# Kernel tuning notes

Measured on AMD Instinct MI355X. Metric: run time of the kernel, lower is better.

The kernel has to match this reference:

```python
import jax, jax.numpy as jnp
import numpy as np
from jax import lax

B, E, DIN = 16, 1024, 128   # batch, num_edges, link_state_dim
P, D = 2048, 128            # num_paths, path_state_dim


def _topology():
    # deterministic ragged paths: lengths in [4,16], at least one of max length 16
    lengths = 4 + (np.arange(P) % 13)
    idx = np.repeat(np.arange(P), lengths).astype(np.int32)          # path id per entry
    seqs = np.concatenate([np.arange(l) for l in lengths]).astype(np.int32)  # position in path
    paths = np.random.RandomState(0).randint(0, E, size=idx.shape[0]).astype(np.int32)
    return paths, idx, seqs


def setup_inputs() -> dict:
    key = jax.random.key(0)
    ks = jax.random.split(key, 8)
    paths, idx, seqs = _topology()
    s_in = 1.0 / np.sqrt(DIN)
    s_h = 1.0 / np.sqrt(D)
    return dict(
        inputs=jax.random.normal(ks[0], (B, E, DIN), jnp.float32),
        W_in=jax.random.normal(ks[1], (DIN, 3 * D), jnp.float32) * s_in,
        W_rec=jax.random.normal(ks[2], (D, 3 * D), jnp.float32) * s_h,
        b_in=jnp.zeros((3 * D,), jnp.float32),
        b_rec=jnp.zeros((3 * D,), jnp.float32),
        wq=jax.random.normal(ks[3], (D, D), jnp.float32) * s_h,
        wk=jax.random.normal(ks[4], (D, D), jnp.float32) * s_h,
        wv=jax.random.normal(ks[5], (D, D), jnp.float32) * s_h,
        paths=paths, idx=idx, seqs=seqs,
    )


def _forward(inputs, W_in, W_rec, b_in, b_rec, wq, wk, wv, paths, idx, seqs, max_len):
    Bc = inputs.shape[0]
    # --- ragged gather -> dense zero-padded tensor [B, P, max_len, DIN] (tf.gather + scatter_nd) ---
    h_tild = inputs[:, paths]                                  # [B, n_entries, DIN]
    link = jnp.zeros((Bc, P, max_len, DIN), inputs.dtype)
    link = link.at[:, idx, seqs].set(h_tild)
    x = link.reshape(Bc * P, max_len, DIN)                     # [BP, L, DIN]
    # --- GRU over time (keras GRUCell default: reset_after=True, tanh/sigmoid) ---
    xg = jnp.einsum('nld,de->lne', x, W_in) + b_in             # [L, BP, 3D]
    h0 = jnp.zeros((Bc * P, D), inputs.dtype)

    def step(h, xg_t):
        hg = h @ W_rec + b_rec                                 # [BP, 3D]
        xz, xr, xh = jnp.split(xg_t, 3, axis=-1)
        hz, hr, hh = jnp.split(hg, 3, axis=-1)
        z = jax.nn.sigmoid(xz + hz)
        r = jax.nn.sigmoid(xr + hr)
        hc = jnp.tanh(xh + r * hh)
        hn = z * h + (1.0 - z) * hc
        return hn, hn

    last, hs = lax.scan(step, h0, xg)                          # last:[BP,D], hs:[L,BP,D]
    hs = jnp.transpose(hs, (1, 0, 2))                          # [BP, L, D]
    # --- single-query QKV attention (raw scores, no softmax, as in source) ---
    key_ = hs @ wk                                             # [BP, L, D]
    val = hs @ wv                                              # [BP, L, D]
    q = last @ wq                                              # [BP, D]
    att = jnp.einsum('nld,nd->nl', key_, q)                    # [BP, L]
    ctx = jnp.einsum('nl,nld->nd', att, val)                   # [BP, D]
    return ctx.reshape(Bc, P, D)


def reference(inputs, W_in, W_rec, b_in, b_rec, wq, wk, wv, paths, idx, seqs):
    max_len = int(np.max(np.asarray(seqs))) + 1                # static (16)
    return _forward(inputs, W_in, W_rec, b_in, b_rec, wq, wk, wv, paths, idx, seqs, max_len)
```

## Files before the change

kernel.cpp:

```cpp
#include <hip/hip_runtime.h>
#include <hip/hip_bf16.h>
#include <cstddef>

#define P_ 2048
#define B_ 16
#define E_ 1024
#define D_ 128
#define L_ 16
#define TD_ 384

#define NEG_L2E (-1.44269504088896340736f)
#define TWO_L2E (2.88539008177792681472f)

typedef _Float16 f16x2 __attribute__((ext_vector_type(2)));
typedef _Float16 f16x8 __attribute__((ext_vector_type(8)));
typedef float    f32x4 __attribute__((ext_vector_type(4)));

__device__ __forceinline__ unsigned short f2h(float x) {
    _Float16 h = (_Float16)x;
    return __builtin_bit_cast(unsigned short, h);
}
__device__ __forceinline__ unsigned pk2(float a, float b) {
    return __builtin_bit_cast(unsigned, __builtin_amdgcn_cvt_pkrtz(a, b));
}
__device__ __forceinline__ float lo16(unsigned u) {
    return (float)__builtin_bit_cast(f16x2, u)[0];
}
__device__ __forceinline__ float hi16(unsigned u) {
    return (float)__builtin_bit_cast(f16x2, u)[1];
}
__device__ __forceinline__ float ex2(float x) {
#if __has_builtin(__builtin_amdgcn_exp2f)
    return __builtin_amdgcn_exp2f(x);
#else
    return exp2f(x);
#endif
}
__device__ __forceinline__ float dot2w(unsigned hu, unsigned qu, float c) {
#if __has_builtin(__builtin_amdgcn_fdot2)
    typedef __fp16 h2v __attribute__((ext_vector_type(2)));
    return __builtin_amdgcn_fdot2(__builtin_bit_cast(h2v, hu),
                                  __builtin_bit_cast(h2v, qu), c, false);
#else
    f16x2 h = __builtin_bit_cast(f16x2, hu), q = __builtin_bit_cast(f16x2, qu);
    return c + (float)h[0] * (float)q[0] + (float)h[1] * (float)q[1];
#endif
}

__device__ __forceinline__ void binv4(const float* __restrict__ d, float* __restrict__ o) {
    float f1 = d[0] * d[1];
    float f2 = f1 * d[2];
    float f3 = f2 * d[3];
    float r  = __builtin_amdgcn_rcpf(f3);
    o[3] = r * f2;
    float t  = r * d[3];
    o[2] = t * f1;
    float u  = t * d[2];
    o[1] = u * d[0];
    o[0] = u * d[1];
}

__device__ __forceinline__ void wf16(const float* __restrict__ src,
                                     unsigned short* __restrict__ dst, int g, int N,
                                     float sc) {
    int lane = g & 63, kt = (g >> 6) & 3, tile = g >> 8;
    int k0 = kt * 32 + (lane >> 4) * 8;
    int c = tile * 16 + (lane & 15);
#pragma unroll
    for (int j = 0; j < 8; ++j)
        dst[(size_t)g * 8 + j] = f2h(src[(size_t)(k0 + j) * N + c] * sc);
}

__device__ __forceinline__ void* hp(void* base, int t, int s, int boff) {
    return (char*)base + ((t * 16 + s) << 8) + (boff ^ ((s & 7) << 4));
}
__device__ __forceinline__ const void* hpc(const void* base, int t, int s, int boff) {
    return (const char*)base + ((t * 16 + s) << 8) + (boff ^ ((s & 7) << 4));
}

__global__ __launch_bounds__(256) void k_prep(const float* __restrict__ W_rec,
                                              const float* __restrict__ W_in,
                                              const float* __restrict__ wq,
                                              const float* __restrict__ wk,
                                              const float* __restrict__ wv,
                                              const int* __restrict__ paths,
                                              int* __restrict__ pt,
                                              unsigned short* __restrict__ WfR,
                                              unsigned short* __restrict__ WfI,
                                              unsigned short* __restrict__ wvf,
                                              float* __restrict__ M) {
    __shared__ float wk_lds[128 * 129];
    __shared__ float wq_row2[2][128];
    int blk = blockIdx.x, tid = threadIdx.x;
    if (blk < 128) {
        int gid = blk * 256 + tid;
        int p = gid >> 4, s = gid & 15;
        int c = p / 13, r = p - c * 13;
        int len = 4 + r;
        int off = 4 * p + 78 * c + (r * (r - 1)) / 2;
        pt[gid] = (s < len) ? paths[off + s] : E_;
        return;
    } else if (blk < 152) {
        int gg = (blk - 128) * 256 + tid;
        wf16(W_rec, WfR, gg, TD_, ((gg >> 8) < 16) ? NEG_L2E : TWO_L2E);
        return;
    } else if (blk < 176) {
        int gg = (blk - 152) * 256 + tid;
        wf16(W_in, WfI, gg, TD_, ((gg >> 8) < 16) ? NEG_L2E : TWO_L2E);
        return;
    } else if (blk < 184) {
        wf16(wv, wvf, (blk - 176) * 256 + tid, 128, 1.f);
        return;
    }
    int j0 = (blk - 184) * 2;
    int d = tid & 127, half = tid >> 7;
    for (int r = half * 64; r < half * 64 + 64; ++r)
        wk_lds[r * 129 + d] = wk[r * 128 + d];
    wq_row2[half][d] = wq[(j0 + half) * 128 + d];
    __syncthreads();
    float acc = 0.f;
    for (int k = 0; k < 128; ++k) acc += wq_row2[half][k] * wk_lds[d * 129 + k];
    M[(j0 + half) * 128 + d] = acc;
}

__global__ __launch_bounds__(256) void k_G(const float* __restrict__ inputs,
                                           const unsigned short* __restrict__ WfI,
                                           const float* __restrict__ b_in,
                                           const float* __restrict__ b_rec,
                                           unsigned short* __restrict__ G2,
                                           const float* __restrict__ M,
                                           unsigned short* __restrict__ Mf) {
    if (blockIdx.x >= 1024) {
        int tb = blockIdx.x - 1024;
        if (tb < 8) {
            wf16(M, Mf, tb * 256 + threadIdx.x, 128, 1.f);
        } else {
            for (int i = threadIdx.x; i < 2048; i += 256) {
                int bx = i >> 7, cc = i & 127;
                size_t base = ((size_t)(bx * (E_ + 1) + E_) * 128 + cc) * 4;
                G2[base]     = f2h((b_in[cc] + b_rec[cc]) * NEG_L2E);
                G2[base + 1] = f2h((b_in[128 + cc] + b_rec[128 + cc]) * NEG_L2E);
                G2[base + 2] = f2h(b_in[256 + cc] * TWO_L2E);
                G2[base + 3] = 0;
            }
        }
        return;
    }
    __shared__ __align__(16) unsigned short a_lds[16][136];
    __shared__ __align__(16) unsigned short g_lds[16][128][4];
    int tid = threadIdx.x, w = tid >> 6, L = tid & 63;
    int l15 = L & 15, q = L >> 4;
    int row0 = blockIdx.x * 16;
    int badd = row0 >> 10;
    {
        int r = tid >> 4, c = (tid & 15) * 8;
        const float4* p = (const float4*)(inputs + (size_t)(row0 + r) * 128 + c);
        float4 v0 = p[0], v1 = p[1];
        uint4 st;
        st.x = pk2(v0.x, v0.y); st.y = pk2(v0.z, v0.w);
        st.z = pk2(v1.x, v1.y); st.w = pk2(v1.z, v1.w);
        *(uint4*)&a_lds[r][c] = st;
    }
    __syncthreads();
    f16x8 af[4];
#pragma unroll
    for (int kt = 0; kt < 4; ++kt)
        af[kt] = *(const f16x8*)&a_lds[l15][kt * 32 + q * 8];
#pragma unroll
    for (int ct = 0; ct < 6; ++ct) {
        int tl = 6 * w + ct;
        f32x4 acc = (f32x4){0.f, 0.f, 0.f, 0.f};
#pragma unroll
        for (int kt = 0; kt < 4; ++kt)
            acc = __builtin_amdgcn_mfma_f32_16x16x32_f16(
                af[kt], *(const f16x8*)(WfI + (size_t)((tl * 4 + kt) * 64 + L) * 8), acc, 0, 0, 0);
        int g  = tl >> 3;
        int dd = (tl & 7) * 16 + l15;
        float sg  = (g < 2) ? NEG_L2E : TWO_L2E;
        float bia = (b_in[tl * 16 + l15] + (g < 2 ? b_rec[tl * 16 + l15] : 0.f)) * sg;
#pragma unroll
        for (int j = 0; j < 4; ++j) {
            int r = q * 4 + j;
            g_lds[r][dd][g] = f2h(acc[j] + bia);
        }
    }
    __syncthreads();
    {
        const uint4* src = (const uint4*)g_lds;
        uint4* dst = (uint4*)(G2 + (size_t)(row0 + badd) * 512);
#pragma unroll
        for (int i = 0; i < 4; ++i) dst[tid + 256 * i] = src[tid + 256 * i];
    }
}

__global__ __launch_bounds__(512, 4) void k_rec(const unsigned short* __restrict__ WfR,
                                                const float* __restrict__ b_rec,
                                                const unsigned short* __restrict__ G2,
                                                const int* __restrict__ pt,
                                                const unsigned short* __restrict__ Mf,
                                                const unsigned short* __restrict__ wvf,
                                                float* __restrict__ out) {
    __shared__ __align__(16) unsigned short hsl[16][16][128];
    __shared__ __align__(16) unsigned short qkb[16][136];
    __shared__ __align__(16) unsigned short svb[16][136];
    __shared__ float attp[2][16][16];
    __shared__ int ofs_lds[16][16];

    int tid = threadIdx.x, w = tid >> 6, L = tid & 63;
    int l15 = L & 15, q = L >> 4;
    int c0 = 16 * w + 4 * q;
    int n0 = blockIdx.x * 16;
    int b  = n0 >> 11;
    int p0 = n0 & (P_ - 1);
    int bb = b * (E_ + 1);

    f16x8 afw[3][4];
#pragma unroll
    for (int g = 0; g < 3; ++g)
#pragma unroll
        for (int kt = 0; kt < 4; ++kt)
            afw[g][kt] = *(const f16x8*)(WfR + (size_t)(((g * 8 + w) * 4 + kt) * 64 + L) * 8);

    if (tid < 256)
        ofs_lds[tid >> 4][tid & 15] = (bb + pt[p0 * L_ + tid]) << 10;

    f32x4 rh4;
#pragma unroll
    for (int j = 0; j < 4; ++j) rh4[j] = b_rec[256 + c0 + j] * TWO_L2E;
    float h_reg[4] = {0.f, 0.f, 0.f, 0.f};
    __syncthreads();

    int ofs[16];
    {
        const uint4* op = (const uint4*)&ofs_lds[l15][0];
        uint4 o0 = op[0], o1 = op[1], o2 = op[2], o3 = op[3];
        ofs[0]  = o0.x; ofs[1]  = o0.y; ofs[2]  = o0.z; ofs[3]  = o0.w;
        ofs[4]  = o1.x; ofs[5]  = o1.y; ofs[6]  = o1.z; ofs[7]  = o1.w;
        ofs[8]  = o2.x; ofs[9]  = o2.y; ofs[10] = o2.z; ofs[11] = o2.w;
        ofs[12] = o3.x; ofs[13] = o3.y; ofs[14] = o3.z; ofs[15] = o3.w;
    }

    const char* g2c = (const char*)G2 + (size_t)c0 * 8;
    uint4 cur0 = *(const uint4*)(g2c + ofs[0]);
    uint4 cur1 = *(const uint4*)(g2c + ofs[0] + 16);

#pragma unroll
    for (int t = 0; t < L_; ++t) {
        uint4 nx0 = cur0, nx1 = cur1;
        if (t < 15) {
            const char* gp = g2c + ofs[t + 1];
            nx0 = *(const uint4*)(gp);
            nx1 = *(const uint4*)(gp + 16);
        }

        float xh[4];
        f32x4 acc[3];
        acc[0][0] = lo16(cur0.x); acc[0][1] = lo16(cur0.z);
        acc[0][2] = lo16(cur1.x); acc[0][3] = lo16(cur1.z);
        acc[1][0] = hi16(cur0.x); acc[1][1] = hi16(cur0.z);
        acc[1][2] = hi16(cur1.x); acc[1][3] = hi16(cur1.z);
        xh[0] = lo16(cur0.y); xh[1] = lo16(cur0.w);
        xh[2] = lo16(cur1.y); xh[3] = lo16(cur1.w);
        acc[2] = rh4;

        if (t > 0) {
            f16x8 hf[4];
#pragma unroll
            for (int kt = 0; kt < 4; ++kt)
                hf[kt] = *(const f16x8*)hpc(hsl, t - 1, l15, kt * 64 + q * 16);
#pragma unroll
            for (int g = 0; g < 3; ++g)
#pragma unroll
                for (int kt = 0; kt < 4; ++kt)
                    acc[g] = __builtin_amdgcn_mfma_f32_16x16x32_f16(afw[g][kt], hf[kt], acc[g], 0, 0, 0);
        }

        float dz[4], dr[4];
#pragma unroll
        for (int j = 0; j < 4; ++j) {
            dz[j] = 1.f + ex2(acc[0][j]);
            dr[j] = 1.f + ex2(acc[1][j]);
        }
        float z4[4], r4[4];
        binv4(dz, z4);
        binv4(dr, r4);
        float dh[4];
#pragma unroll
        for (int j = 0; j < 4; ++j)
            dh[j] = 1.f + ex2(fminf(xh[j] + r4[j] * acc[2][j], 30.f));
        float y4[4];
        binv4(dh, y4);
        float hn[4];
#pragma unroll
        for (int j = 0; j < 4; ++j) {
            float hc = 1.f - 2.f * y4[j];
            hn[j] = hc + z4[j] * (h_reg[j] - hc);
            h_reg[j] = hn[j];
        }
        uint2 st;
        st.x = pk2(hn[0], hn[1]); st.y = pk2(hn[2], hn[3]);
        *(uint2*)hp(hsl, t, l15, c0 * 2) = st;
        cur0 = nx0; cur1 = nx1;

        __builtin_amdgcn_wave_barrier();
        __builtin_amdgcn_s_waitcnt(0xC07F);
        __builtin_amdgcn_s_barrier();
        __builtin_amdgcn_wave_barrier();
    }

    {
        f16x8 hf[4];
#pragma unroll
        for (int kt = 0; kt < 4; ++kt)
            hf[kt] = *(const f16x8*)hpc(hsl, 15, l15, kt * 64 + q * 16);
        f32x4 a = (f32x4){0.f, 0.f, 0.f, 0.f};
#pragma unroll
        for (int kt = 0; kt < 4; ++kt)
            a = __builtin_amdgcn_mfma_f32_16x16x32_f16(
                *(const f16x8*)(Mf + (size_t)((w * 4 + kt) * 64 + L) * 8), hf[kt], a, 0, 0, 0);
        uint2 st;
        st.x = pk2(a[0], a[1]); st.y = pk2(a[2], a[3]);
        *(uint2*)&qkb[l15][c0] = st;
    }
    __syncthreads();

    {
        int s = tid & 15, l = (tid >> 4) & 15, half = tid >> 8;
        const uint4* qr = (const uint4*)&qkb[s][half * 64];
        float a = 0.f;
#pragma unroll
        for (int k8 = 0; k8 < 8; ++k8) {
            uint4 hh = *(const uint4*)hpc(hsl, l, s, half * 128 + k8 * 16);
            uint4 qq = qr[k8];
            a = dot2w(hh.x, qq.x, a); a = dot2w(hh.y, qq.y, a);
            a = dot2w(hh.z, qq.z, a); a = dot2w(hh.w, qq.w, a);
        }
        attp[half][s][l] = a;
    }
    __syncthreads();

    {
        int s = tid >> 5, d0 = (tid & 31) * 4;
        float v[4] = {0.f, 0.f, 0.f, 0.f};
#pragma unroll
        for (int l = 0; l < 16; ++l) {
            float a = attp[0][s][l] + attp[1][s][l];
            uint2 hu = *(const uint2*)hpc(hsl, l, s, d0 * 2);
            v[0] += a * lo16(hu.x); v[1] += a * hi16(hu.x);
            v[2] += a * lo16(hu.y); v[3] += a * hi16(hu.y);
        }
        uint2 st;
        st.x = pk2(v[0], v[1]); st.y = pk2(v[2], v[3]);
        *(uint2*)&svb[s][d0] = st;
    }
    __syncthreads();

    {
        f16x8 sf[4];
#pragma unroll
        for (int kt = 0; kt < 4; ++kt)
            sf[kt] = *(const f16x8*)&svb[l15][kt * 32 + q * 8];
        f32x4 a = (f32x4){0.f, 0.f, 0.f, 0.f};
#pragma unroll
        for (int kt = 0; kt < 4; ++kt)
            a = __builtin_amdgcn_mfma_f32_16x16x32_f16(
                *(const f16x8*)(wvf + (size_t)((w * 4 + kt) * 64 + L) * 8), sf[kt], a, 0, 0, 0);
        *(f32x4*)&out[(size_t)(n0 + l15) * D_ + c0] = a;
    }
}

extern "C" void kernel_launch(void* const* d_in, const int* in_sizes, int n_in,
                              void* d_out, int out_size, void* d_ws, size_t ws_size,
                              hipStream_t stream) {
    const float* inputs = (const float*)d_in[0];
    const float* W_in   = (const float*)d_in[1];
    const float* W_rec  = (const float*)d_in[2];
    const float* b_in   = (const float*)d_in[3];
    const float* b_rec  = (const float*)d_in[4];
    const float* wq     = (const float*)d_in[5];
    const float* wk     = (const float*)d_in[6];
    const float* wvp    = (const float*)d_in[7];
    const int* paths    = (const int*)d_in[8];

    const size_t off_pt  = 0;
    const size_t off_WfR = off_pt  + (size_t)P_ * L_ * 4;
    const size_t off_WfI = off_WfR + (size_t)24 * 256 * 16;
    const size_t off_Mf  = off_WfI + (size_t)24 * 256 * 16;
    const size_t off_wvf = off_Mf  + (size_t)8 * 256 * 16;
    const size_t off_M   = off_wvf + (size_t)8 * 256 * 16;
    const size_t off_G2  = off_M   + (size_t)128 * 128 * 4;
    char* ws = (char*)d_ws;
    int* pt             = (int*)(ws + off_pt);
    unsigned short* WfR = (unsigned short*)(ws + off_WfR);
    unsigned short* WfI = (unsigned short*)(ws + off_WfI);
    unsigned short* Mf  = (unsigned short*)(ws + off_Mf);
    unsigned short* wvf = (unsigned short*)(ws + off_wvf);
    float* M            = (float*)(ws + off_M);
    unsigned short* G2  = (unsigned short*)(ws + off_G2);
    float* out = (float*)d_out;

    k_prep<<<dim3(248), dim3(256), 0, stream>>>(W_rec, W_in, wq, wk, wvp, paths,
                                                pt, WfR, WfI, wvf, M);
    k_G<<<dim3(1024 + 8 + 1), dim3(256), 0, stream>>>(inputs, WfI, b_in, b_rec,
                                                      G2, M, Mf);
    k_rec<<<dim3(B_ * P_ / 16), dim3(512), 0, stream>>>(WfR, b_rec, G2, pt,
                                                        Mf, wvf, out);
}
```

Baseline: 173.6 us.

## Fuse input projection into recurrent kernel, gathering fp16 inputs per step

Removes the separate k_G kernel that precomputed per-edge input gate projections (G2). The prep kernel now converts inputs to an fp16 copy with a zero row per batch for padding, and writes Mf directly in MFMA layout. The recurrent kernel gathers the raw fp16 input rows and computes the input projection with extra MFMAs each step, with biases added in registers. This drops one launch and the G2 round trip, but the sequential loop now does twice the MFMA work and holds both weight sets in registers, which adds register pressure.

```diff
diff --git a/kernel.cpp b/kernel.cpp
--- a/kernel.cpp
+++ b/kernel.cpp
@@ -83,12 +83,14 @@
                                               const float* __restrict__ wq,
                                               const float* __restrict__ wk,
                                               const float* __restrict__ wv,
+                                              const float* __restrict__ inputs,
                                               const int* __restrict__ paths,
                                               int* __restrict__ pt,
                                               unsigned short* __restrict__ WfR,
                                               unsigned short* __restrict__ WfI,
                                               unsigned short* __restrict__ wvf,
-                                              float* __restrict__ M) {
+                                              unsigned short* __restrict__ Mf,
+                                              unsigned short* __restrict__ X2) {
     __shared__ float wk_lds[128 * 129];
     __shared__ float wq_row2[2][128];
     int blk = blockIdx.x, tid = threadIdx.x;
@@ -111,6 +113,20 @@
     } else if (blk < 184) {
         wf16(wv, wvf, (blk - 176) * 256 + tid, 128, 1.f);
         return;
+    } else if (blk >= 248) {
+        int g = (blk - 248) * 16 + (tid >> 4);
+        int seg = tid & 15;
+        int b = g / 1025;
+        int e = g - b * 1025;
+        uint4 st = (uint4){0u, 0u, 0u, 0u};
+        if (e < 1024) {
+            const float4* p = (const float4*)(inputs + (size_t)(g - b) * 128 + seg * 8);
+            float4 v0 = p[0], v1 = p[1];
+            st.x = pk2(v0.x, v0.y); st.y = pk2(v0.z, v0.w);
+            st.z = pk2(v1.x, v1.y); st.w = pk2(v1.z, v1.w);
+        }
+        *(uint4*)(X2 + (size_t)g * 128 + seg * 8) = st;
+        return;
     }
     int j0 = (blk - 184) * 2;
     int d = tid & 127, half = tid >> 7;
@@ -120,82 +136,19 @@
     __syncthreads();
     float acc = 0.f;
     for (int k = 0; k < 128; ++k) acc += wq_row2[half][k] * wk_lds[d * 129 + k];
-    M[(j0 + half) * 128 + d] = acc;
-}
-
-__global__ __launch_bounds__(256) void k_G(const float* __restrict__ inputs,
-                                           const unsigned short* __restrict__ WfI,
-                                           const float* __restrict__ b_in,
-                                           const float* __restrict__ b_rec,
-                                           unsigned short* __restrict__ G2,
-                                           const float* __restrict__ M,
-                                           unsigned short* __restrict__ Mf) {
-    if (blockIdx.x >= 1024) {
-        int tb = blockIdx.x - 1024;
-        if (tb < 8) {
-            wf16(M, Mf, tb * 256 + threadIdx.x, 128, 1.f);
-        } else {
-            for (int i = threadIdx.x; i < 2048; i += 256) {
-                int bx = i >> 7, cc = i & 127;
-                size_t base = ((size_t)(bx * (E_ + 1) + E_) * 128 + cc) * 4;
-                G2[base]     = f2h((b_in[cc] + b_rec[cc]) * NEG_L2E);
-                G2[base + 1] = f2h((b_in[128 + cc] + b_rec[128 + cc]) * NEG_L2E);
-                G2[base + 2] = f2h(b_in[256 + cc] * TWO_L2E);
-                G2[base + 3] = 0;
-            }
-        }
-        return;
-    }
-    __shared__ __align__(16) unsigned short a_lds[16][136];
-    __shared__ __align__(16) unsigned short g_lds[16][128][4];
-    int tid = threadIdx.x, w = tid >> 6, L = tid & 63;
-    int l15 = L & 15, q = L >> 4;
-    int row0 = blockIdx.x * 16;
-    int badd = row0 >> 10;
-    {
-        int r = tid >> 4, c = (tid & 15) * 8;
-        const float4* p = (const float4*)(inputs + (size_t)(row0 + r) * 128 + c);
-        float4 v0 = p[0], v1 = p[1];
-        uint4 st;
-        st.x = pk2(v0.x, v0.y); st.y = pk2(v0.z, v0.w);
-        st.z = pk2(v1.x, v1.y); st.w = pk2(v1.z, v1.w);
-        *(uint4*)&a_lds[r][c] = st;
-    }
-    __syncthreads();
-    f16x8 af[4];
-#pragma unroll
-    for (int kt = 0; kt < 4; ++kt)
-        af[kt] = *(const f16x8*)&a_lds[l15][kt * 32 + q * 8];
-#pragma unroll
-    for (int ct = 0; ct < 6; ++ct) {
-        int tl = 6 * w + ct;
-        f32x4 acc = (f32x4){0.f, 0.f, 0.f, 0.f};
-#pragma unroll
-        for (int kt = 0; kt < 4; ++kt)
-            acc = __builtin_amdgcn_mfma_f32_16x16x32_f16(
-                af[kt], *(const f16x8*)(WfI + (size_t)((tl * 4 + kt) * 64 + L) * 8), acc, 0, 0, 0);
-        int g  = tl >> 3;
-        int dd = (tl & 7) * 16 + l15;
-        float sg  = (g < 2) ? NEG_L2E : TWO_L2E;
-        float bia = (b_in[tl * 16 + l15] + (g < 2 ? b_rec[tl * 16 + l15] : 0.f)) * sg;
-#pragma unroll
-        for (int j = 0; j < 4; ++j) {
-            int r = q * 4 + j;
-            g_lds[r][dd][g] = f2h(acc[j] + bia);
-        }
-    }
-    __syncthreads();
-    {
-        const uint4* src = (const uint4*)g_lds;
-        uint4* dst = (uint4*)(G2 + (size_t)(row0 + badd) * 512);
-#pragma unroll
-        for (int i = 0; i < 4; ++i) dst[tid + 256 * i] = src[tid + 256 * i];
+    {
+        int r = j0 + half;
+        int tile = d >> 4, kt = r >> 5;
+        int ln = ((r >> 3) & 3) * 16 + (d & 15), jj = r & 7;
+        Mf[((size_t)(tile * 4 + kt) * 64 + ln) * 8 + jj] = f2h(acc);
     }
 }
 
 __global__ __launch_bounds__(512, 4) void k_rec(const unsigned short* __restrict__ WfR,
+                                                const unsigned short* __restrict__ WfI,
+                                                const float* __restrict__ b_in,
                                                 const float* __restrict__ b_rec,
-                                                const unsigned short* __restrict__ G2,
+                                                const unsigned short* __restrict__ X2,
                                                 const int* __restrict__ pt,
                                                 const unsigned short* __restrict__ Mf,
                                                 const unsigned short* __restrict__ wvf,
@@ -214,54 +167,44 @@
     int p0 = n0 & (P_ - 1);
     int bb = b * (E_ + 1);
 
-    f16x8 afw[3][4];
+    f16x8 afwR[3][4], afwI[3][4];
 #pragma unroll
     for (int g = 0; g < 3; ++g)
 #pragma unroll
-        for (int kt = 0; kt < 4; ++kt)
-            afw[g][kt] = *(const f16x8*)(WfR + (size_t)(((g * 8 + w) * 4 + kt) * 64 + L) * 8);
+        for (int kt = 0; kt < 4; ++kt) {
+            afwR[g][kt] = *(const f16x8*)(WfR + (size_t)(((g * 8 + w) * 4 + kt) * 64 + L) * 8);
+            afwI[g][kt] = *(const f16x8*)(WfI + (size_t)(((g * 8 + w) * 4 + kt) * 64 + L) * 8);
+        }
 
     if (tid < 256)
-        ofs_lds[tid >> 4][tid & 15] = (bb + pt[p0 * L_ + tid]) << 10;
-
-    f32x4 rh4;
-#pragma unroll
-    for (int j = 0; j < 4; ++j) rh4[j] = b_rec[256 + c0 + j] * TWO_L2E;
+        ofs_lds[tid >> 4][tid & 15] = (bb + pt[p0 * L_ + tid]) << 8;
+
+    f32x4 bz4, br4, bx4, rh4;
+#pragma unroll
+    for (int j = 0; j < 4; ++j) {
+        bz4[j] = (b_in[c0 + j] + b_rec[c0 + j]) * NEG_L2E;
+        br4[j] = (b_in[128 + c0 + j] + b_rec[128 + c0 + j]) * NEG_L2E;
+        bx4[j] = b_in[256 + c0 + j] * TWO_L2E;
+        rh4[j] = b_rec[256 + c0 + j] * TWO_L2E;
+    }
     float h_reg[4] = {0.f, 0.f, 0.f, 0.f};
     __syncthreads();
 
-    int ofs[16];
-    {
-        const uint4* op = (const uint4*)&ofs_lds[l15][0];
-        uint4 o0 = op[0], o1 = op[1], o2 = op[2], o3 = op[3];
-        ofs[0]  = o0.x; ofs[1]  = o0.y; ofs[2]  = o0.z; ofs[3]  = o0.w;
-        ofs[4]  = o1.x; ofs[5]  = o1.y; ofs[6]  = o1.z; ofs[7]  = o1.w;
-        ofs[8]  = o2.x; ofs[9]  = o2.y; ofs[10] = o2.z; ofs[11] = o2.w;
-        ofs[12] = o3.x; ofs[13] = o3.y; ofs[14] = o3.z; ofs[15] = o3.w;
-    }
-
-    const char* g2c = (const char*)G2 + (size_t)c0 * 8;
-    uint4 cur0 = *(const uint4*)(g2c + ofs[0]);
-    uint4 cur1 = *(const uint4*)(g2c + ofs[0] + 16);
+    const char* xb = (const char*)X2 + q * 16;
+    int ocur = ofs_lds[l15][0];
 
 #pragma unroll
     for (int t = 0; t < L_; ++t) {
-        uint4 nx0 = cur0, nx1 = cur1;
-        if (t < 15) {
-            const char* gp = g2c + ofs[t + 1];
-            nx0 = *(const uint4*)(gp);
-            nx1 = *(const uint4*)(gp + 16);
-        }
-
-        float xh[4];
-        f32x4 acc[3];
-        acc[0][0] = lo16(cur0.x); acc[0][1] = lo16(cur0.z);
-        acc[0][2] = lo16(cur1.x); acc[0][3] = lo16(cur1.z);
-        acc[1][0] = hi16(cur0.x); acc[1][1] = hi16(cur0.z);
-        acc[1][2] = hi16(cur1.x); acc[1][3] = hi16(cur1.z);
-        xh[0] = lo16(cur0.y); xh[1] = lo16(cur0.w);
-        xh[2] = lo16(cur1.y); xh[3] = lo16(cur1.w);
-        acc[2] = rh4;
+        const char* xp = xb + ocur;
+        f16x8 xf[4];
+        xf[0] = *(const f16x8*)(xp);
+        xf[1] = *(const f16x8*)(xp + 64);
+        xf[2] = *(const f16x8*)(xp + 128);
+        xf[3] = *(const f16x8*)(xp + 192);
+        int onext = ocur;
+        if (t < 15) onext = ofs_lds[l15][t + 1];
+
+        f32x4 az = bz4, ar = br4, ax = bx4, ah = rh4;
 
         if (t > 0) {
             f16x8 hf[4];
@@ -269,17 +212,24 @@
             for (int kt = 0; kt < 4; ++kt)
                 hf[kt] = *(const f16x8*)hpc(hsl, t - 1, l15, kt * 64 + q * 16);
 #pragma unroll
-            for (int g = 0; g < 3; ++g)
-#pragma unroll
-                for (int kt = 0; kt < 4; ++kt)
-                    acc[g] = __builtin_amdgcn_mfma_f32_16x16x32_f16(afw[g][kt], hf[kt], acc[g], 0, 0, 0);
+            for (int kt = 0; kt < 4; ++kt) {
+                az = __builtin_amdgcn_mfma_f32_16x16x32_f16(afwR[0][kt], hf[kt], az, 0, 0, 0);
+                ar = __builtin_amdgcn_mfma_f32_16x16x32_f16(afwR[1][kt], hf[kt], ar, 0, 0, 0);
+                ah = __builtin_amdgcn_mfma_f32_16x16x32_f16(afwR[2][kt], hf[kt], ah, 0, 0, 0);
+            }
+        }
+#pragma unroll
+        for (int kt = 0; kt < 4; ++kt) {
+            az = __builtin_amdgcn_mfma_f32_16x16x32_f16(afwI[0][kt], xf[kt], az, 0, 0, 0);
+            ar = __builtin_amdgcn_mfma_f32_16x16x32_f16(afwI[1][kt], xf[kt], ar, 0, 0, 0);
+            ax = __builtin_amdgcn_mfma_f32_16x16x32_f16(afwI[2][kt], xf[kt], ax, 0, 0, 0);
         }
 
         float dz[4], dr[4];
 #pragma unroll
         for (int j = 0; j < 4; ++j) {
-            dz[j] = 1.f + ex2(acc[0][j]);
-            dr[j] = 1.f + ex2(acc[1][j]);
+            dz[j] = 1.f + ex2(az[j]);
+            dr[j] = 1.f + ex2(ar[j]);
         }
         float z4[4], r4[4];
         binv4(dz, z4);
@@ -287,7 +237,7 @@
         float dh[4];
 #pragma unroll
         for (int j = 0; j < 4; ++j)
-            dh[j] = 1.f + ex2(fminf(xh[j] + r4[j] * acc[2][j], 30.f));
+            dh[j] = 1.f + ex2(fminf(ax[j] + r4[j] * ah[j], 30.f));
         float y4[4];
         binv4(dh, y4);
         float hn[4];
@@ -300,7 +250,7 @@
         uint2 st;
         st.x = pk2(hn[0], hn[1]); st.y = pk2(hn[2], hn[3]);
         *(uint2*)hp(hsl, t, l15, c0 * 2) = st;
-        cur0 = nx0; cur1 = nx1;
+        ocur = onext;
 
         __builtin_amdgcn_wave_barrier();
         __builtin_amdgcn_s_waitcnt(0xC07F);
@@ -387,22 +337,19 @@
     const size_t off_WfI = off_WfR + (size_t)24 * 256 * 16;
     const size_t off_Mf  = off_WfI + (size_t)24 * 256 * 16;
     const size_t off_wvf = off_Mf  + (size_t)8 * 256 * 16;
-    const size_t off_M   = off_wvf + (size_t)8 * 256 * 16;
-    const size_t off_G2  = off_M   + (size_t)128 * 128 * 4;
+    const size_t off_X2  = off_wvf + (size_t)8 * 256 * 16;
     char* ws = (char*)d_ws;
     int* pt             = (int*)(ws + off_pt);
     unsigned short* WfR = (unsigned short*)(ws + off_WfR);
     unsigned short* WfI = (unsigned short*)(ws + off_WfI);
     unsigned short* Mf  = (unsigned short*)(ws + off_Mf);
     unsigned short* wvf = (unsigned short*)(ws + off_wvf);
-    float* M            = (float*)(ws + off_M);
-    unsigned short* G2  = (unsigned short*)(ws + off_G2);
+    unsigned short* X2  = (unsigned short*)(ws + off_X2);
     float* out = (float*)d_out;
 
-    k_prep<<<dim3(248), dim3(256), 0, stream>>>(W_rec, W_in, wq, wk, wvp, paths,
-                                                pt, WfR, WfI, wvf, M);
-    k_G<<<dim3(1024 + 8 + 1), dim3(256), 0, stream>>>(inputs, WfI, b_in, b_rec,
-                                                      G2, M, Mf);
-    k_rec<<<dim3(B_ * P_ / 16), dim3(512), 0, stream>>>(WfR, b_rec, G2, pt,
-                                                        Mf, wvf, out);
-}
+    k_prep<<<dim3(248 + 1025), dim3(256), 0, stream>>>(W_rec, W_in, wq, wk, wvp,
+                                                       inputs, paths, pt,
+                                                       WfR, WfI, wvf, Mf, X2);
+    k_rec<<<dim3(B_ * P_ / 16), dim3(512), 0, stream>>>(WfR, WfI, b_in, b_rec,
+                                                        X2, pt, Mf, wvf, out);
+}
```

After: 595.4 us. 3.43x slower.
